# Kernel tuning notes

Hardware: AMD Instinct MI355X
Metric: run time of the kernel (lower is better)

Reference implementation:

```python
import jax, jax.numpy as jnp
import numpy as np

NEG_SLOPE = 0.2  # PyG GATConv default negative_slope


def gat_layer(x, src, dst, W, a_src, a_dst, bias, concat, N):
    """PyG GATConv: h = xW; e_ij = LeakyReLU(a_src.h_j + a_dst.h_i);
    alpha = segment-softmax over incoming edges of i; out_i = sum_j alpha_ij h_j."""
    H, C = a_src.shape
    h = (x @ W).reshape(N, H, C)                      # [N,H,C]
    alpha_s = jnp.einsum('nhc,hc->nh', h, a_src)      # [N,H]
    alpha_d = jnp.einsum('nhc,hc->nh', h, a_dst)      # [N,H]
    e = jax.nn.leaky_relu(alpha_s[src] + alpha_d[dst], NEG_SLOPE)  # [E,H]
    # numerically-stable segment softmax over destination nodes
    m = jax.ops.segment_max(e, dst, num_segments=N)   # [N,H]
    e = jnp.exp(e - m[dst])
    denom = jax.ops.segment_sum(e, dst, num_segments=N)
    alpha = e / (denom[dst] + 1e-16)                  # [E,H]
    msg = h[src] * alpha[:, :, None]                  # [E,H,C]
    out = jax.ops.segment_sum(msg, dst, num_segments=N)  # [N,H,C]
    out = out.reshape(N, H * C) if concat else out.mean(axis=1)
    return out + bias


def setup_inputs() -> dict:
    key = jax.random.key(0)
    ks = jax.random.split(key, 12)
    N, E, F_IN, C, H = 50000, 800000, 512, 32, 8
    s = 0.05
    x = jax.random.normal(ks[0], (N, F_IN), dtype=jnp.float32)
    edge_index = jax.random.randint(ks[1], (2, E), 0, N, dtype=jnp.int64)
    W1 = jax.random.normal(ks[2], (F_IN, H * C), dtype=jnp.float32) * s
    as1 = jax.random.normal(ks[3], (H, C), dtype=jnp.float32) * s
    ad1 = jax.random.normal(ks[4], (H, C), dtype=jnp.float32) * s
    b1 = jnp.zeros((H * C,), dtype=jnp.float32)
    W2 = jax.random.normal(ks[5], (H * C, H * C), dtype=jnp.float32) * s
    as2 = jax.random.normal(ks[6], (H, C), dtype=jnp.float32) * s
    ad2 = jax.random.normal(ks[7], (H, C), dtype=jnp.float32) * s
    b2 = jnp.zeros((C,), dtype=jnp.float32)
    Wp = jax.random.normal(ks[8], (C, 1), dtype=jnp.float32) * s
    bp = jnp.zeros((1,), dtype=jnp.float32)
    return {"edge_index": edge_index, "x": x, "W1": W1, "as1": as1, "ad1": ad1,
            "b1": b1, "W2": W2, "as2": as2, "ad2": ad2, "b2": b2,
            "Wp": Wp, "bp": bp}


def reference(edge_index, x, W1, as1, ad1, b1, W2, as2, ad2, b2, Wp, bp):
    N = x.shape[0]
    # PyG GATConv adds self-loops by default
    loops = jnp.arange(N, dtype=edge_index.dtype)
    src = jnp.concatenate([edge_index[0], loops])
    dst = jnp.concatenate([edge_index[1], loops])
    h = gat_layer(x, src, dst, W1, as1, ad1, b1, concat=True, N=N)
    h = jax.nn.relu(h)
    # F.dropout(training=self.training) is identity in eval mode
    h = gat_layer(h, src, dst, W2, as2, ad2, b2, concat=False, N=N)
    return jax.nn.sigmoid(h @ Wp + bp)   # [N,1]
```

## Files before the change

kernel.cpp:

```cpp
#include <hip/hip_runtime.h>
#include <math.h>

#define H_HEADS 8
#define C_DIM   32
#define HC      256
#define F_IN    512
#define NEG_SLOPE 0.2f

typedef __attribute__((ext_vector_type(8))) short    bf16x8;
typedef __attribute__((ext_vector_type(4))) short    s16x4;
typedef __attribute__((ext_vector_type(4))) float    f32x4;
typedef __attribute__((ext_vector_type(2))) float    f32x2;
typedef __attribute__((ext_vector_type(8))) _Float16 h16x8;

__device__ __forceinline__ short f2bf(float f) {
    union { float f; unsigned u; } v; v.f = f;
    unsigned r = v.u + 0x7FFF + ((v.u >> 16) & 1);
    return (short)(r >> 16);
}

__device__ __forceinline__ bf16x8 cvt8(float4 a, float4 b) {
    union { bf16x8 v; unsigned u[4]; } r;
    asm("v_cvt_pk_bf16_f32 %0, %1, %2" : "=v"(r.u[0]) : "v"(a.x), "v"(a.y));
    asm("v_cvt_pk_bf16_f32 %0, %1, %2" : "=v"(r.u[1]) : "v"(a.z), "v"(a.w));
    asm("v_cvt_pk_bf16_f32 %0, %1, %2" : "=v"(r.u[2]) : "v"(b.x), "v"(b.y));
    asm("v_cvt_pk_bf16_f32 %0, %1, %2" : "=v"(r.u[3]) : "v"(b.z), "v"(b.w));
    return r.v;
}

__device__ __forceinline__ void gl2lds16(const short* g, short* l) {
    __builtin_amdgcn_global_load_lds(
        (const __attribute__((address_space(1))) void*)g,
        (__attribute__((address_space(3))) void*)l, 16, 0, 0);
}

__global__ void wfrag_kernel(const float* __restrict__ W, short* __restrict__ Wf, int K)
{
    int tid = blockIdx.x * 256 + threadIdx.x;
    if (tid >= K * HC) return;
    int j  = tid & 7;
    int l  = (tid >> 3) & 63;
    int nb = (tid >> 9) & 15;
    int s  = tid >> 13;
    int k  = s * 32 + (l >> 4) * 8 + j;
    int n  = nb * 16 + (l & 15);
    Wf[tid] = f2bf(W[(size_t)k * HC + n]);
}

template<bool ABF16>
__global__ __launch_bounds__(256, 2) void gemm_mfma(const void* __restrict__ Aptr,
    const short* __restrict__ Bf, unsigned char* __restrict__ h8,
    const float* __restrict__ a_s, const float* __restrict__ a_d,
    float* __restrict__ alpha_s, float* __restrict__ alpha_d, int M, int K)
{
    __shared__ short Bs[2][16384];
    __shared__ float Als[1024], Ald[1024];

    const int tid  = threadIdx.x;
    const int w    = tid >> 6;
    const int lane = tid & 63;
    const int quad = lane >> 4;
    const int ml   = lane & 15;
    const int wm   = w & 1;
    const int wn   = w >> 1;
    const int bm   = blockIdx.x * 128;

    f32x4 acc[4][8];
    #pragma unroll
    for (int ff = 0; ff < 4; ++ff)
        #pragma unroll
        for (int nb = 0; nb < 8; ++nb) acc[ff][nb] = (f32x4){0.f, 0.f, 0.f, 0.f};

    const float* A32 = (const float*)Aptr;
    const short* A16 = (const short*)Aptr;
    const int nph = K >> 6;

    const float* ap32[4];
    const short* ap16[4];
    #pragma unroll
    for (int ff = 0; ff < 4; ++ff) {
        int row = bm + wm * 64 + ff * 16 + ml;
        int rl  = row < M ? row : M - 1;
        if (ABF16) ap16[ff] = A16 + (size_t)rl * K + quad * 8;
        else       ap32[ff] = A32 + (size_t)rl * K + quad * 8;
    }

    {
        const short* g = Bf + (size_t)w * 4096 + lane * 8;
        short* l = &Bs[0][w * 4096];
        #pragma unroll
        for (int c = 0; c < 8; ++c) gl2lds16(g + c * 512, l + c * 512);
    }

    float4 pf[4][4];
    bf16x8 pb[4][2];
    if (ABF16) {
        #pragma unroll
        for (int ff = 0; ff < 4; ++ff)
            #pragma unroll
            for (int kk = 0; kk < 2; ++kk)
                pb[ff][kk] = *(const bf16x8*)(ap16[ff] + kk * 32);
    } else {
        #pragma unroll
        for (int ff = 0; ff < 4; ++ff)
            #pragma unroll
            for (int kk = 0; kk < 2; ++kk) {
                pf[ff][2 * kk]     = *(const float4*)(ap32[ff] + kk * 32);
                pf[ff][2 * kk + 1] = *(const float4*)(ap32[ff] + kk * 32 + 4);
            }
    }

    for (int p = 0; p < nph; ++p) {
        __syncthreads();

        if (p + 1 < nph) {
            const short* g = Bf + (size_t)(p + 1) * 16384 + w * 4096 + lane * 8;
            short* l = &Bs[(p + 1) & 1][w * 4096];
            #pragma unroll
            for (int c = 0; c < 8; ++c) gl2lds16(g + c * 512, l + c * 512);
        }

        bf16x8 af[2][4];
        if (ABF16) {
            #pragma unroll
            for (int kk = 0; kk < 2; ++kk)
                #pragma unroll
                for (int ff = 0; ff < 4; ++ff) af[kk][ff] = pb[ff][kk];
        } else {
            #pragma unroll
            for (int kk = 0; kk < 2; ++kk)
                #pragma unroll
                for (int ff = 0; ff < 4; ++ff)
                    af[kk][ff] = cvt8(pf[ff][2 * kk], pf[ff][2 * kk + 1]);
        }

        if (p + 1 < nph) {
            const int kb = (p + 1) * 64;
            if (ABF16) {
                #pragma unroll
                for (int ff = 0; ff < 4; ++ff)
                    #pragma unroll
                    for (int kk = 0; kk < 2; ++kk)
                        pb[ff][kk] = *(const bf16x8*)(ap16[ff] + kb + kk * 32);
            } else {
                #pragma unroll
                for (int ff = 0; ff < 4; ++ff)
                    #pragma unroll
                    for (int kk = 0; kk < 2; ++kk) {
                        pf[ff][2 * kk]     = *(const float4*)(ap32[ff] + kb + kk * 32);
                        pf[ff][2 * kk + 1] = *(const float4*)(ap32[ff] + kb + kk * 32 + 4);
                    }
            }
        }

        const short* bbase = &Bs[p & 1][(wn * 8) * 512 + lane * 8];
        #pragma unroll
        for (int kk = 0; kk < 2; ++kk) {
            #pragma unroll
            for (int nb = 0; nb < 8; ++nb) {
                bf16x8 bfr = *(const bf16x8*)(bbase + kk * 8192 + nb * 512);
                #pragma unroll
                for (int ff = 0; ff < 4; ++ff)
                    acc[ff][nb] = __builtin_amdgcn_mfma_f32_16x16x32_bf16(
                        af[kk][ff], bfr, acc[ff][nb], 0, 0, 0);
            }
        }
    }

    float as_v[8], ad_v[8];
    #pragma unroll
    for (int nb = 0; nb < 8; ++nb) {
        const int col = wn * 128 + nb * 16 + ml;
        as_v[nb] = a_s[col];
        ad_v[nb] = a_d[col];
    }

    #pragma unroll
    for (int ff = 0; ff < 4; ++ff) {
        #pragma unroll
        for (int r = 0; r < 4; ++r) {
            const int rl  = wm * 64 + ff * 16 + quad * 4 + r;
            const int row = bm + rl;

            if (row < M) {
                unsigned char* hrow = h8 + (size_t)row * HC + wn * 128;
                #pragma unroll
                for (int i = 0; i < 4; ++i) {
                    int pk = __builtin_amdgcn_cvt_pk_fp8_f32(
                        acc[ff][2 * i][r], acc[ff][2 * i + 1][r], 0, false);
                    hrow[(2 * i) * 16 + ml]     = (unsigned char)(pk & 0xFF);
                    hrow[(2 * i + 1) * 16 + ml] = (unsigned char)((pk >> 8) & 0xFF);
                }
            }

            float hs[4], hd[4];
            #pragma unroll
            for (int q = 0; q < 4; ++q) {
                hs[q] = acc[ff][2 * q][r] * as_v[2 * q] + acc[ff][2 * q + 1][r] * as_v[2 * q + 1];
                hd[q] = acc[ff][2 * q][r] * ad_v[2 * q] + acc[ff][2 * q + 1][r] * ad_v[2 * q + 1];
            }
            #pragma unroll
            for (int off = 1; off < 16; off <<= 1) {
                #pragma unroll
                for (int q = 0; q < 4; ++q) {
                    hs[q] += __shfl_xor(hs[q], off);
                    hd[q] += __shfl_xor(hd[q], off);
                }
            }
            if (ml == 0) {
                #pragma unroll
                for (int q = 0; q < 4; ++q) {
                    Als[rl * 8 + wn * 4 + q] = hs[q];
                    Ald[rl * 8 + wn * 4 + q] = hd[q];
                }
            }
        }
    }
    __syncthreads();
    #pragma unroll
    for (int k = 0; k < 4; ++k) {
        int idx = tid + k * 256;
        int rl = idx >> 3, q = idx & 7;
        int row = bm + rl;
        if (row < M) {
            alpha_s[(size_t)row * H_HEADS + q] = Als[idx];
            alpha_d[(size_t)row * H_HEADS + q] = Ald[idx];
        }
    }
}

__global__ __launch_bounds__(256) void wcalc_kernel(const int2* __restrict__ es,
    const float* __restrict__ alpha_s, const float* __restrict__ alpha_d,
    _Float16* __restrict__ wq, int P)
{
    int p = blockIdx.x * 256 + threadIdx.x;
    if (p >= P) return;
    int2 sd = es[p];
    const float4* as = (const float4*)(alpha_s + (size_t)sd.x * H_HEADS);
    const float4* ad = (const float4*)(alpha_d + (size_t)sd.y * H_HEADS);
    float4 s0 = as[0], s1 = as[1], d0 = ad[0], d1 = ad[1];
    float e[8] = {s0.x + d0.x, s0.y + d0.y, s0.z + d0.z, s0.w + d0.w,
                  s1.x + d1.x, s1.y + d1.y, s1.z + d1.z, s1.w + d1.w};
    h16x8 o;
    #pragma unroll
    for (int h = 0; h < 8; ++h) {
        float v = e[h] > 0.f ? e[h] : NEG_SLOPE * e[h];
        o[h] = (_Float16)__expf(v);
    }
    *(h16x8*)(wq + (size_t)p * H_HEADS) = o;
}

__global__ void zero_int(int* __restrict__ p, int n)
{
    int i = blockIdx.x * 256 + threadIdx.x;
    if (i < n) p[i] = 0;
}

__global__ void hist_kernel(const int* __restrict__ ei, int E, int N,
                            int* __restrict__ cnt)
{
    int e = blockIdx.x * 256 + threadIdx.x;
    if (e < E) atomicAdd(&cnt[ei[E + e]], 1);
    else if (e < E + N) atomicAdd(&cnt[e - E], 1);
}

__global__ __launch_bounds__(256) void scan_sum(const int* __restrict__ cnt, int n,
                                                int* __restrict__ chunk_sum)
{
    __shared__ int lds[256];
    int b = blockIdx.x, t = threadIdx.x;
    int base = b * 1024 + t * 4;
    int s = 0;
    #pragma unroll
    for (int j = 0; j < 4; ++j) { int i = base + j; if (i < n) s += cnt[i]; }
    lds[t] = s; __syncthreads();
    for (int off = 128; off > 0; off >>= 1) {
        if (t < off) lds[t] += lds[t + off];
        __syncthreads();
    }
    if (t == 0) chunk_sum[b] = lds[0];
}

__global__ void scan_top(const int* __restrict__ chunk_sum, int nch,
                         int* __restrict__ chunk_off, int* __restrict__ row_ptr,
                         int n_nodes)
{
    int t = threadIdx.x;
    int v = (t < nch) ? chunk_sum[t] : 0;
    int inc = v;
    #pragma unroll
    for (int off = 1; off < 64; off <<= 1) {
        int u = __shfl_up(inc, off);
        if (t >= off) inc += u;
    }
    if (t < nch) chunk_off[t] = inc - v;
    if (t == 63) row_ptr[n_nodes] = inc;
}

__global__ __launch_bounds__(256) void scan_local(const int* __restrict__ cnt, int n,
    const int* __restrict__ chunk_off, int* __restrict__ row_ptr)
{
    __shared__ int lds[256];
    int b = blockIdx.x, t = threadIdx.x;
    int base = b * 1024 + t * 4;
    int v[4]; int s = 0;
    #pragma unroll
    for (int j = 0; j < 4; ++j) { int i = base + j; v[j] = (i < n) ? cnt[i] : 0; s += v[j]; }
    lds[t] = s; __syncthreads();
    for (int off = 1; off < 256; off <<= 1) {
        int u = (t >= off) ? lds[t - off] : 0;
        __syncthreads();
        lds[t] += u;
        __syncthreads();
    }
    int run = lds[t] - s + chunk_off[b];
    #pragma unroll
    for (int j = 0; j < 4; ++j) {
        int i = base + j;
        if (i < n) row_ptr[i] = run;
        run += v[j];
    }
}

__global__ void scatter_kernel(const int* __restrict__ ei, int E, int N,
    const int* __restrict__ row_ptr, int* __restrict__ fill, int2* __restrict__ es)
{
    int e = blockIdx.x * 256 + threadIdx.x;
    int src, dst;
    if (e < E)          { src = ei[e]; dst = ei[E + e]; }
    else if (e < E + N) { src = dst = e - E; }
    else return;
    int pos = row_ptr[dst] + atomicAdd(&fill[dst], 1);
    es[pos] = make_int2(src, dst);
}

__global__ __launch_bounds__(256) void agg1_kernel(const unsigned* __restrict__ h8,
    const _Float16* __restrict__ wq, const int* __restrict__ row_ptr,
    const int2* __restrict__ es, const float* __restrict__ bias,
    short* __restrict__ z_bf, int N)
{
    const int l = threadIdx.x & 63;
    const int i = blockIdx.x * 4 + (threadIdx.x >> 6);
    if (i >= N) return;
    const int hh = l >> 3;
    const int beg = row_ptr[i], end = row_ptr[i + 1];
    f32x4 acc = {0.f, 0.f, 0.f, 0.f};
    float dsum = 0.f;
    int p = beg;
    for (; p + 7 < end; p += 8) {
        int s[8]; float w[8]; unsigned hv[8];
        #pragma unroll
        for (int u = 0; u < 8; ++u) s[u] = es[p + u].x;
        #pragma unroll
        for (int u = 0; u < 8; ++u) w[u] = (float)wq[(size_t)(p + u) * 8 + hh];
        #pragma unroll
        for (int u = 0; u < 8; ++u) hv[u] = h8[(size_t)s[u] * 64 + l];
        #pragma unroll
        for (int u = 0; u < 8; ++u) {
            f32x2 lo = __builtin_amdgcn_cvt_pk_f32_fp8(hv[u], false);
            f32x2 hi = __builtin_amdgcn_cvt_pk_f32_fp8(hv[u], true);
            acc[0] = fmaf(w[u], lo[0], acc[0]);
            acc[1] = fmaf(w[u], lo[1], acc[1]);
            acc[2] = fmaf(w[u], hi[0], acc[2]);
            acc[3] = fmaf(w[u], hi[1], acc[3]);
            dsum += w[u];
        }
    }
    for (; p < end; ++p) {
        int s0 = es[p].x;
        float w0 = (float)wq[(size_t)p * 8 + hh];
        unsigned hv = h8[(size_t)s0 * 64 + l];
        f32x2 lo = __builtin_amdgcn_cvt_pk_f32_fp8(hv, false);
        f32x2 hi = __builtin_amdgcn_cvt_pk_f32_fp8(hv, true);
        acc[0] = fmaf(w0, lo[0], acc[0]);
        acc[1] = fmaf(w0, lo[1], acc[1]);
        acc[2] = fmaf(w0, hi[0], acc[2]);
        acc[3] = fmaf(w0, hi[1], acc[3]);
        dsum += w0;
    }
    float inv = 1.f / (dsum + 1e-16f);
    s16x4 pk;
    #pragma unroll
    for (int j = 0; j < 4; ++j) {
        float z = acc[j] * inv + bias[4 * l + j];
        pk[j] = f2bf(z > 0.f ? z : 0.f);
    }
    *(s16x4*)(z_bf + (size_t)i * HC + 4 * l) = pk;
}

__global__ __launch_bounds__(256) void agg2_kernel(const unsigned* __restrict__ h8,
    const _Float16* __restrict__ wq, const int* __restrict__ row_ptr,
    const int2* __restrict__ es, const float* __restrict__ b2,
    const float* __restrict__ Wp, const float* __restrict__ bp,
    float* __restrict__ out, int N)
{
    const int l = threadIdx.x & 63;
    const int i = blockIdx.x * 4 + (threadIdx.x >> 6);
    if (i >= N) return;
    const int hh = l >> 3;
    const int beg = row_ptr[i], end = row_ptr[i + 1];
    f32x4 acc = {0.f, 0.f, 0.f, 0.f};
    float dsum = 0.f;
    int p = beg;
    for (; p + 7 < end; p += 8) {
        int s[8]; float w[8]; unsigned hv[8];
        #pragma unroll
        for (int u = 0; u < 8; ++u) s[u] = es[p + u].x;
        #pragma unroll
        for (int u = 0; u < 8; ++u) w[u] = (float)wq[(size_t)(p + u) * 8 + hh];
        #pragma unroll
        for (int u = 0; u < 8; ++u) hv[u] = h8[(size_t)s[u] * 64 + l];
        #pragma unroll
        for (int u = 0; u < 8; ++u) {
            f32x2 lo = __builtin_amdgcn_cvt_pk_f32_fp8(hv[u], false);
            f32x2 hi = __builtin_amdgcn_cvt_pk_f32_fp8(hv[u], true);
            acc[0] = fmaf(w[u], lo[0], acc[0]);
            acc[1] = fmaf(w[u], lo[1], acc[1]);
            acc[2] = fmaf(w[u], hi[0], acc[2]);
            acc[3] = fmaf(w[u], hi[1], acc[3]);
            dsum += w[u];
        }
    }
    for (; p < end; ++p) {
        int s0 = es[p].x;
        float w0 = (float)wq[(size_t)p * 8 + hh];
        unsigned hv = h8[(size_t)s0 * 64 + l];
        f32x2 lo = __builtin_amdgcn_cvt_pk_f32_fp8(hv, false);
        f32x2 hi = __builtin_amdgcn_cvt_pk_f32_fp8(hv, true);
        acc[0] = fmaf(w0, lo[0], acc[0]);
        acc[1] = fmaf(w0, lo[1], acc[1]);
        acc[2] = fmaf(w0, hi[0], acc[2]);
        acc[3] = fmaf(w0, hi[1], acc[3]);
        dsum += w0;
    }
    float inv = 1.f / (dsum + 1e-16f);
    int cc = (4 * l) & 31;
    float partial = 0.f;
    #pragma unroll
    for (int j = 0; j < 4; ++j) partial = fmaf(acc[j] * inv, Wp[cc + j], partial);
    if (l < 8) {
        #pragma unroll
        for (int j = 0; j < 4; ++j) partial = fmaf(8.f * b2[4 * l + j], Wp[4 * l + j], partial);
    }
    #pragma unroll
    for (int off = 32; off > 0; off >>= 1) partial += __shfl_xor(partial, off);
    if (l == 0) out[i] = 1.f / (1.f + __expf(-(0.125f * partial + bp[0])));
}

extern "C" void kernel_launch(void* const* d_in, const int* in_sizes, int n_in,
                              void* d_out, int out_size, void* d_ws, size_t ws_size,
                              hipStream_t stream)
{
    const int*   ei  = (const int*)d_in[0];
    const float* x   = (const float*)d_in[1];
    const float* W1  = (const float*)d_in[2];
    const float* as1 = (const float*)d_in[3];
    const float* ad1 = (const float*)d_in[4];
    const float* b1  = (const float*)d_in[5];
    const float* W2  = (const float*)d_in[6];
    const float* as2 = (const float*)d_in[7];
    const float* ad2 = (const float*)d_in[8];
    const float* b2  = (const float*)d_in[9];
    const float* Wp  = (const float*)d_in[10];
    const float* bp  = (const float*)d_in[11];
    float* out = (float*)d_out;

    const int E = in_sizes[0] / 2;
    const int N = in_sizes[1] / F_IN;
    const int ET = E + N;

    float*         asb = (float*)d_ws;
    float*         adb = asb + (size_t)N * H_HEADS;
    unsigned char* h8  = (unsigned char*)(adb + (size_t)N * H_HEADS);
    short*         z1b = (short*)(h8 + (size_t)N * HC);
    short*         Wf1 = z1b + (size_t)N * HC;
    short*         Wf2 = Wf1 + (size_t)F_IN * HC;
    _Float16*      wq  = (_Float16*)(Wf2 + (size_t)HC * HC);
    int2*          es  = (int2*)(wq + (size_t)ET * H_HEADS);
    int* cnt       = (int*)(es + ET);
    int* fill      = cnt + N;
    int* row_ptr   = fill + N;
    int* chunk_off = row_ptr + N + 1;
    int* chunk_sum = chunk_off + 64;

    const int NCH = (N + 1023) / 1024;
    const int MB  = (N + 127) / 128;
    const int NB4 = (N + 3) / 4;

    zero_int<<<(2 * N + 255) / 256, 256, 0, stream>>>(cnt, 2 * N);
    hist_kernel<<<(ET + 255) / 256, 256, 0, stream>>>(ei, E, N, cnt);
    scan_sum<<<NCH, 256, 0, stream>>>(cnt, N, chunk_sum);
    scan_top<<<1, 64, 0, stream>>>(chunk_sum, NCH, chunk_off, row_ptr, N);
    scan_local<<<NCH, 256, 0, stream>>>(cnt, N, chunk_off, row_ptr);
    scatter_kernel<<<(ET + 255) / 256, 256, 0, stream>>>(ei, E, N, row_ptr, fill, es);

    wfrag_kernel<<<(F_IN * HC + 255) / 256, 256, 0, stream>>>(W1, Wf1, F_IN);
    wfrag_kernel<<<(HC * HC + 255) / 256, 256, 0, stream>>>(W2, Wf2, HC);

    gemm_mfma<false><<<MB, 256, 0, stream>>>(x, Wf1, h8, as1, ad1, asb, adb, N, F_IN);
    wcalc_kernel<<<(ET + 255) / 256, 256, 0, stream>>>(es, asb, adb, wq, ET);
    agg1_kernel<<<NB4, 256, 0, stream>>>((const unsigned*)h8, wq, row_ptr, es, b1, z1b, N);

    gemm_mfma<true><<<MB, 256, 0, stream>>>(z1b, Wf2, h8, as2, ad2, asb, adb, N, HC);
    wcalc_kernel<<<(ET + 255) / 256, 256, 0, stream>>>(es, asb, adb, wq, ET);
    agg2_kernel<<<NB4, 256, 0, stream>>>((const unsigned*)h8, wq, row_ptr, es, b2, Wp, bp, out, N);
}
```

Baseline: 421.7 us.

## Stage the whole B column-half in LDS and split GEMM blocks by column

The feature GEMM is restructured so each block covers 256 rows and one 128-column half of the output. It loads that half's entire weight panel for all of K into LDS up front, then runs the K loop with one barrier instead of a double-buffered per-phase pipeline. This removes the per-iteration barriers and the LDS double buffering. In exchange, each A row is now read by two blocks, which doubles global A traffic (notably the fp32 x input). The larger LDS footprint also limits occupancy to one block per CU.

```diff
diff --git a/kernel.cpp b/kernel.cpp
--- a/kernel.cpp
+++ b/kernel.cpp
@@ -47,13 +47,14 @@
     Wf[tid] = f2bf(W[(size_t)k * HC + n]);
 }
 
-template<bool ABF16>
-__global__ __launch_bounds__(256, 2) void gemm_mfma(const void* __restrict__ Aptr,
+template<bool ABF16, int NKS>
+__global__ __launch_bounds__(256, 1) void gemm_mfma(const void* __restrict__ Aptr,
     const short* __restrict__ Bf, unsigned char* __restrict__ h8,
     const float* __restrict__ a_s, const float* __restrict__ a_d,
-    float* __restrict__ alpha_s, float* __restrict__ alpha_d, int M, int K)
-{
-    __shared__ short Bs[2][16384];
+    float* __restrict__ alpha_s, float* __restrict__ alpha_d, int M)
+{
+    constexpr int K = NKS * 32;
+    __shared__ short Bs[NKS * 4096];
     __shared__ float Als[1024], Ald[1024];
 
     const int tid  = threadIdx.x;
@@ -61,116 +62,86 @@
     const int lane = tid & 63;
     const int quad = lane >> 4;
     const int ml   = lane & 15;
-    const int wm   = w & 1;
-    const int wn   = w >> 1;
-    const int bm   = blockIdx.x * 128;
-
-    f32x4 acc[4][8];
-    #pragma unroll
-    for (int ff = 0; ff < 4; ++ff)
-        #pragma unroll
-        for (int nb = 0; nb < 8; ++nb) acc[ff][nb] = (f32x4){0.f, 0.f, 0.f, 0.f};
+    const int cb   = blockIdx.x & 1;
+    const int bm   = (blockIdx.x >> 1) * 256;
 
     const float* A32 = (const float*)Aptr;
     const short* A16 = (const short*)Aptr;
-    const int nph = K >> 6;
 
     const float* ap32[4];
     const short* ap16[4];
     #pragma unroll
     for (int ff = 0; ff < 4; ++ff) {
-        int row = bm + wm * 64 + ff * 16 + ml;
+        int row = bm + w * 64 + ff * 16 + ml;
         int rl  = row < M ? row : M - 1;
         if (ABF16) ap16[ff] = A16 + (size_t)rl * K + quad * 8;
         else       ap32[ff] = A32 + (size_t)rl * K + quad * 8;
     }
 
-    {
-        const short* g = Bf + (size_t)w * 4096 + lane * 8;
-        short* l = &Bs[0][w * 4096];
-        #pragma unroll
-        for (int c = 0; c < 8; ++c) gl2lds16(g + c * 512, l + c * 512);
-    }
-
-    float4 pf[4][4];
-    bf16x8 pb[4][2];
+    float4 pf[4][2];
+    bf16x8 pb[4];
     if (ABF16) {
         #pragma unroll
-        for (int ff = 0; ff < 4; ++ff)
-            #pragma unroll
-            for (int kk = 0; kk < 2; ++kk)
-                pb[ff][kk] = *(const bf16x8*)(ap16[ff] + kk * 32);
+        for (int ff = 0; ff < 4; ++ff) pb[ff] = *(const bf16x8*)(ap16[ff]);
     } else {
         #pragma unroll
-        for (int ff = 0; ff < 4; ++ff)
-            #pragma unroll
-            for (int kk = 0; kk < 2; ++kk) {
-                pf[ff][2 * kk]     = *(const float4*)(ap32[ff] + kk * 32);
-                pf[ff][2 * kk + 1] = *(const float4*)(ap32[ff] + kk * 32 + 4);
-            }
-    }
-
-    for (int p = 0; p < nph; ++p) {
-        __syncthreads();
-
-        if (p + 1 < nph) {
-            const short* g = Bf + (size_t)(p + 1) * 16384 + w * 4096 + lane * 8;
-            short* l = &Bs[(p + 1) & 1][w * 4096];
-            #pragma unroll
-            for (int c = 0; c < 8; ++c) gl2lds16(g + c * 512, l + c * 512);
-        }
-
-        bf16x8 af[2][4];
+        for (int ff = 0; ff < 4; ++ff) {
+            pf[ff][0] = *(const float4*)(ap32[ff]);
+            pf[ff][1] = *(const float4*)(ap32[ff] + 4);
+        }
+    }
+
+    for (int ci = w; ci < NKS * 8; ci += 4) {
+        const short* g = Bf + (size_t)(ci >> 3) * 8192 + cb * 4096 + (ci & 7) * 512 + lane * 8;
+        gl2lds16(g, &Bs[ci * 512]);
+    }
+
+    f32x4 acc[4][8];
+    #pragma unroll
+    for (int ff = 0; ff < 4; ++ff)
+        #pragma unroll
+        for (int nb = 0; nb < 8; ++nb) acc[ff][nb] = (f32x4){0.f, 0.f, 0.f, 0.f};
+
+    __syncthreads();
+
+    #pragma unroll
+    for (int ks = 0; ks < NKS; ++ks) {
+        bf16x8 af[4];
         if (ABF16) {
             #pragma unroll
-            for (int kk = 0; kk < 2; ++kk)
+            for (int ff = 0; ff < 4; ++ff) af[ff] = pb[ff];
+            if (ks + 1 < NKS) {
                 #pragma unroll
-                for (int ff = 0; ff < 4; ++ff) af[kk][ff] = pb[ff][kk];
+                for (int ff = 0; ff < 4; ++ff)
+                    pb[ff] = *(const bf16x8*)(ap16[ff] + (ks + 1) * 32);
+            }
         } else {
             #pragma unroll
-            for (int kk = 0; kk < 2; ++kk)
+            for (int ff = 0; ff < 4; ++ff) af[ff] = cvt8(pf[ff][0], pf[ff][1]);
+            if (ks + 1 < NKS) {
                 #pragma unroll
-                for (int ff = 0; ff < 4; ++ff)
-                    af[kk][ff] = cvt8(pf[ff][2 * kk], pf[ff][2 * kk + 1]);
-        }
-
-        if (p + 1 < nph) {
-            const int kb = (p + 1) * 64;
-            if (ABF16) {
-                #pragma unroll
-                for (int ff = 0; ff < 4; ++ff)
-                    #pragma unroll
-                    for (int kk = 0; kk < 2; ++kk)
-                        pb[ff][kk] = *(const bf16x8*)(ap16[ff] + kb + kk * 32);
-            } else {
-                #pragma unroll
-                for (int ff = 0; ff < 4; ++ff)
-                    #pragma unroll
-                    for (int kk = 0; kk < 2; ++kk) {
-                        pf[ff][2 * kk]     = *(const float4*)(ap32[ff] + kb + kk * 32);
-                        pf[ff][2 * kk + 1] = *(const float4*)(ap32[ff] + kb + kk * 32 + 4);
-                    }
-            }
-        }
-
-        const short* bbase = &Bs[p & 1][(wn * 8) * 512 + lane * 8];
-        #pragma unroll
-        for (int kk = 0; kk < 2; ++kk) {
+                for (int ff = 0; ff < 4; ++ff) {
+                    pf[ff][0] = *(const float4*)(ap32[ff] + (ks + 1) * 32);
+                    pf[ff][1] = *(const float4*)(ap32[ff] + (ks + 1) * 32 + 4);
+                }
+            }
+        }
+
+        const short* bbase = &Bs[ks * 4096 + lane * 8];
+        #pragma unroll
+        for (int nb = 0; nb < 8; ++nb) {
+            bf16x8 bfr = *(const bf16x8*)(bbase + nb * 512);
             #pragma unroll
-            for (int nb = 0; nb < 8; ++nb) {
-                bf16x8 bfr = *(const bf16x8*)(bbase + kk * 8192 + nb * 512);
-                #pragma unroll
-                for (int ff = 0; ff < 4; ++ff)
-                    acc[ff][nb] = __builtin_amdgcn_mfma_f32_16x16x32_bf16(
-                        af[kk][ff], bfr, acc[ff][nb], 0, 0, 0);
-            }
+            for (int ff = 0; ff < 4; ++ff)
+                acc[ff][nb] = __builtin_amdgcn_mfma_f32_16x16x32_bf16(
+                    af[ff], bfr, acc[ff][nb], 0, 0, 0);
         }
     }
 
     float as_v[8], ad_v[8];
     #pragma unroll
     for (int nb = 0; nb < 8; ++nb) {
-        const int col = wn * 128 + nb * 16 + ml;
+        const int col = cb * 128 + nb * 16 + ml;
         as_v[nb] = a_s[col];
         ad_v[nb] = a_d[col];
     }
@@ -179,11 +150,11 @@
     for (int ff = 0; ff < 4; ++ff) {
         #pragma unroll
         for (int r = 0; r < 4; ++r) {
-            const int rl  = wm * 64 + ff * 16 + quad * 4 + r;
+            const int rl  = w * 64 + ff * 16 + quad * 4 + r;
             const int row = bm + rl;
 
             if (row < M) {
-                unsigned char* hrow = h8 + (size_t)row * HC + wn * 128;
+                unsigned char* hrow = h8 + (size_t)row * HC + cb * 128;
                 #pragma unroll
                 for (int i = 0; i < 4; ++i) {
                     int pk = __builtin_amdgcn_cvt_pk_fp8_f32(
@@ -210,21 +181,21 @@
             if (ml == 0) {
                 #pragma unroll
                 for (int q = 0; q < 4; ++q) {
-                    Als[rl * 8 + wn * 4 + q] = hs[q];
-                    Ald[rl * 8 + wn * 4 + q] = hd[q];
+                    Als[rl * 4 + q] = hs[q];
+                    Ald[rl * 4 + q] = hd[q];
                 }
             }
         }
     }
     __syncthreads();
     #pragma unroll
-    for (int k = 0; k < 4; ++k) {
-        int idx = tid + k * 256;
-        int rl = idx >> 3, q = idx & 7;
+    for (int k2 = 0; k2 < 4; ++k2) {
+        int idx = tid + k2 * 256;
+        int rl = idx >> 2, q = idx & 3;
         int row = bm + rl;
         if (row < M) {
-            alpha_s[(size_t)row * H_HEADS + q] = Als[idx];
-            alpha_d[(size_t)row * H_HEADS + q] = Ald[idx];
+            alpha_s[(size_t)row * H_HEADS + cb * 4 + q] = Als[idx];
+            alpha_d[(size_t)row * H_HEADS + cb * 4 + q] = Ald[idx];
         }
     }
 }
@@ -484,7 +455,7 @@
     int* chunk_sum = chunk_off + 64;
 
     const int NCH = (N + 1023) / 1024;
-    const int MB  = (N + 127) / 128;
+    const int MB  = ((N + 255) / 256) * 2;
     const int NB4 = (N + 3) / 4;
 
     zero_int<<<(2 * N + 255) / 256, 256, 0, stream>>>(cnt, 2 * N);
@@ -497,11 +468,11 @@
     wfrag_kernel<<<(F_IN * HC + 255) / 256, 256, 0, stream>>>(W1, Wf1, F_IN);
     wfrag_kernel<<<(HC * HC + 255) / 256, 256, 0, stream>>>(W2, Wf2, HC);
 
-    gemm_mfma<false><<<MB, 256, 0, stream>>>(x, Wf1, h8, as1, ad1, asb, adb, N, F_IN);
+    gemm_mfma<false, 16><<<MB, 256, 0, stream>>>(x, Wf1, h8, as1, ad1, asb, adb, N);
     wcalc_kernel<<<(ET + 255) / 256, 256, 0, stream>>>(es, asb, adb, wq, ET);
     agg1_kernel<<<NB4, 256, 0, stream>>>((const unsigned*)h8, wq, row_ptr, es, b1, z1b, N);
 
-    gemm_mfma<true><<<MB, 256, 0, stream>>>(z1b, Wf2, h8, as2, ad2, asb, adb, N, HC);
+    gemm_mfma<true, 8><<<MB, 256, 0, stream>>>(z1b, Wf2, h8, as2, ad2, asb, adb, N);
     wcalc_kernel<<<(ET + 255) / 256, 256, 0, stream>>>(es, asb, adb, wq, ET);
     agg2_kernel<<<NB4, 256, 0, stream>>>((const unsigned*)h8, wq, row_ptr, es, b2, Wp, bp, out, N);
 }
```

Result: slower. 438.7 us (+4.0%).
